# Kernel optimization log

Hardware: AMD Instinct MI355X
Metric: run time of the kernel (lower is better)

## Reference

```python
import jax, jax.numpy as jnp
import numpy as np

B_BOUND = 3.0
K = 10
SCALE_DIM = 8
TOTAL_DIM = 16
HID = 50
N = 262144
TD = TOTAL_DIM - SCALE_DIM  # transform_dim


def setup_inputs() -> dict:
    key = jax.random.key(0)
    ks = jax.random.split(key, 7)
    s = 0.1  # small init so softmax/softplus params stay well-conditioned
    return {
        "x": jax.random.normal(ks[0], (N, TOTAL_DIM), dtype=jnp.float32),
        "w0": s * jax.random.normal(ks[1], (SCALE_DIM, HID), dtype=jnp.float32),
        "b0": jnp.zeros((HID,), jnp.float32),
        "w1": s * jax.random.normal(ks[2], (HID, HID), dtype=jnp.float32),
        "b1": jnp.zeros((HID,), jnp.float32),
        "ww": s * jax.random.normal(ks[3], (HID, TD * K), dtype=jnp.float32),
        "bw": jnp.zeros((TD * K,), jnp.float32),
        "wh": s * jax.random.normal(ks[4], (HID, TD * K), dtype=jnp.float32),
        "bh": jnp.zeros((TD * K,), jnp.float32),
        "wd": s * jax.random.normal(ks[5], (HID, TD * (K - 1)), dtype=jnp.float32),
        "bd": jnp.zeros((TD * (K - 1),), jnp.float32),
    }


def _spline_forward(x, w0, b0, w1, b1, ww, bw, wh, bh, wd, bd):
    B = B_BOUND
    zd = x[:, :SCALE_DIM]          # conditioner input [N, d]
    u = x[:, SCALE_DIM:]           # values to transform [N, D]
    n, D = u.shape

    h = jnp.tanh(zd @ w0 + b0)
    h = jnp.tanh(h @ w1 + b1)

    theta_w = jax.nn.softmax((2.0 * B * (h @ ww + bw)).reshape(n, D, K), axis=-1)
    theta_h = jax.nn.softmax((2.0 * B * (h @ wh + bh)).reshape(n, D, K), axis=-1)
    theta_d = jax.nn.softplus((h @ wd + bd).reshape(n, D, K - 1))

    # Bin edges in [-B, B] via cumsum of normalized widths/heights
    xe = jnp.concatenate(
        [jnp.full((n, D, 1), -B, u.dtype), -B + 2.0 * B * jnp.cumsum(theta_w, axis=-1)], axis=-1)  # [n,D,K+1]
    ye = jnp.concatenate(
        [jnp.full((n, D, 1), -B, u.dtype), -B + 2.0 * B * jnp.cumsum(theta_h, axis=-1)], axis=-1)
    # Knot derivatives: boundary derivatives fixed to 1 (linear tails)
    ones = jnp.ones((n, D, 1), u.dtype)
    d = jnp.concatenate([ones, theta_d, ones], axis=-1)  # [n,D,K+1]

    widths = xe[..., 1:] - xe[..., :-1]
    heights = ye[..., 1:] - ye[..., :-1]

    inside = (u > -B) & (u < B)
    uc = jnp.clip(u, -B, B)
    # per-element bin search
    idx = jnp.clip(jnp.sum((uc[..., None] >= xe[..., :-1]).astype(jnp.int32), axis=-1) - 1, 0, K - 1)
    idx = idx[..., None]
    take = lambda a: jnp.take_along_axis(a, idx, axis=-1)[..., 0]

    xk, yk = take(xe[..., :-1]), take(ye[..., :-1])
    wk, hk = take(widths), take(heights)
    dk, dk1 = take(d[..., :-1]), take(d[..., 1:])

    sk = hk / wk
    xi = (uc - xk) / wk
    om = 1.0 - xi
    denom = sk + (dk1 + dk - 2.0 * sk) * xi * om
    y = yk + hk * (sk * xi * xi + dk * xi * om) / denom
    logdet = 2.0 * jnp.log(sk) + jnp.log(dk1 * xi * xi + 2.0 * sk * xi * om + dk * om * om) - 2.0 * jnp.log(denom)

    zD = jnp.where(inside, y, u)
    ld = jnp.where(inside, logdet, 0.0)
    return jnp.concatenate([zd, zD], axis=1), jnp.sum(ld)


def reference(x, w0, b0, w1, b1, ww, bw, wh, bh, wd, bd):
    return _spline_forward(x, w0, b0, w1, b1, ww, bw, wh, bh, wd, bd)
```

## Files before the change

kernel.cpp:

```cpp
#include <hip/hip_runtime.h>

#define NROWS 262144
#define KK 10
#define BB 3.0f
#define SROW 132
#define HS 84
#define SEGF16 (16 * SROW)
#define SENT 0.54132485f

typedef _Float16 v8h __attribute__((ext_vector_type(8)));
typedef _Float16 v4h __attribute__((ext_vector_type(4)));
typedef float v4f __attribute__((ext_vector_type(4)));

#define W0_OFF 0
#define W1_OFF 256
#define WC_OFF 768
#define FRAG_TOTAL 2816
#define SLOTS_OFF (FRAG_TOTAL * 4)

#if __has_builtin(__builtin_amdgcn_exp2f)
__device__ __forceinline__ float ex2(float x) { return __builtin_amdgcn_exp2f(x); }
#else
__device__ __forceinline__ float ex2(float x) { return __expf(0.6931471805599453f * x); }
#endif
#if __has_builtin(__builtin_amdgcn_rcpf)
__device__ __forceinline__ float frcp(float x) { return __builtin_amdgcn_rcpf(x); }
#else
__device__ __forceinline__ float frcp(float x) { return __fdividef(1.0f, x); }
#endif

#define LOG2E 1.4426950408889634f
#define C6 (6.0f * LOG2E)
#define CT (2.0f * LOG2E)

__device__ __forceinline__ float fast_tanh(float a) {
    const float e = ex2(CT * a);
    return fmaf(-2.0f, frcp(e + 1.0f), 1.0f);
}

__device__ __forceinline__ float softplus1(float v) {
    return fmaxf(v, 0.0f) + __logf(1.0f + ex2(-LOG2E * fabsf(v)));
}

__device__ __forceinline__ void spline_task(
    const _Float16* __restrict__ sg, int base, float ud, int g, int d,
    float* __restrict__ out, float& ldacc)
{
    float vals[32];
    #pragma unroll
    for (int blk = 0; blk < 8; ++blk) {
        const v4h p = *(const v4h*)&sg[base + blk * 4];
        vals[4 * blk + 0] = (float)p[0];
        vals[4 * blk + 1] = (float)p[1];
        vals[4 * blk + 2] = (float)p[2];
        vals[4 * blk + 3] = (float)p[3];
    }

    float mw = vals[0];
    #pragma unroll
    for (int i = 1; i < KK; ++i) mw = fmaxf(mw, vals[i]);
    const float mw8 = mw * C6;
    float sw = 0.0f;
    #pragma unroll
    for (int i = 0; i < KK; ++i) { vals[i] = ex2(fmaf(vals[i], C6, -mw8)); sw += vals[i]; }
    const float invw = frcp(sw);

    float mh = vals[10];
    #pragma unroll
    for (int i = 1; i < KK; ++i) mh = fmaxf(mh, vals[10 + i]);
    const float mh8 = mh * C6;
    float sh = 0.0f;
    #pragma unroll
    for (int i = 0; i < KK; ++i) { vals[10 + i] = ex2(fmaf(vals[10 + i], C6, -mh8)); sh += vals[10 + i]; }
    const float invh = frcp(sh);

    const float uc = fminf(fmaxf(ud, -BB), BB);
    const bool inside = (ud > -BB) && (ud < BB);

    float cw = 0.0f, ch = 0.0f;
    float xprev = -BB, yprev = -BB, rprev = SENT;
    float xk = -BB, yk = -BB, wk = 1.0f, hk2 = 1.0f, rdk = SENT, rdk1 = SENT;
    #pragma unroll
    for (int i = 0; i < KK; ++i) {
        cw += vals[i] * invw;
        ch += vals[10 + i] * invh;
        const float xnext = fmaf(6.0f, cw, -BB);
        const float ynext = fmaf(6.0f, ch, -BB);
        const float rnext = (i == KK - 1) ? SENT : vals[20 + i];
        const bool c = (i == 0) || (uc >= xprev);
        if (c) { xk = xprev; yk = yprev; wk = xnext - xprev; hk2 = ynext - yprev; rdk = rprev; rdk1 = rnext; }
        xprev = xnext; yprev = ynext; rprev = rnext;
    }
    const float dk = softplus1(rdk);
    const float dk1 = softplus1(rdk1);

    const float rwk = frcp(wk);
    const float sk = hk2 * rwk;
    const float xi = (uc - xk) * rwk;
    const float om = 1.0f - xi;
    const float denom = sk + (dk1 + dk - 2.0f * sk) * xi * om;
    const float rden = frcp(denom);
    const float ynum = sk * xi * xi + dk * xi * om;
    const float yv = yk + hk2 * ynum * rden;
    const float larg = dk1 * xi * xi + 2.0f * sk * xi * om + dk * om * om;
    const float ldet = __logf(sk * sk * larg * rden * rden);

    out[g * 16 + 8 + d] = inside ? yv : ud;
    ldacc += inside ? ldet : 0.0f;
}

__global__ __launch_bounds__(256) void nsf_prep(
    const float* __restrict__ w0, const float* __restrict__ b0,
    const float* __restrict__ w1, const float* __restrict__ b1,
    const float* __restrict__ ww, const float* __restrict__ bw,
    const float* __restrict__ wh, const float* __restrict__ bh,
    const float* __restrict__ wd, const float* __restrict__ bd,
    v8h* __restrict__ wsv, float* __restrict__ wsf)
{
    const int t = blockIdx.x * 256 + threadIdx.x;
    if (t < 64) wsf[SLOTS_OFF + t] = 0.0f;
    if (t >= FRAG_TOTAL) return;

    v8h v;
    #pragma unroll
    for (int j = 0; j < 8; ++j) v[j] = (_Float16)0.0f;

    if (t < W1_OFF) {
        const int tile = t >> 6, lane = t & 63, q = lane >> 4, n = tile * 16 + (lane & 15);
        if (n < 50) {
            #pragma unroll
            for (int j = 0; j < 8; ++j) {
                const int k = q * 8 + j;
                if (k < 8)       v[j] = (_Float16)w0[k * 50 + n];
                else if (k == 8) v[j] = (_Float16)b0[n];
            }
        }
    } else if (t < WC_OFF) {
        int p = t - W1_OFF;
        const int step = p >> 8; p &= 255;
        const int tile = p >> 6, lane = p & 63, q = lane >> 4, n = tile * 16 + (lane & 15);
        if (n < 50) {
            #pragma unroll
            for (int j = 0; j < 8; ++j) {
                const int k = step * 32 + q * 8 + j;
                if (k < 50)       v[j] = (_Float16)w1[k * 50 + n];
                else if (k == 50) v[j] = (_Float16)b1[n];
            }
        }
    } else {
        int p = t - WC_OFF;
        const int step = p >> 10; p &= 1023;
        const int tile = p >> 6, lane = p & 63, q = lane >> 4;
        const int cp = tile * 16 + (lane & 15);
        const int d = cp >> 5, jj = cp & 31;
        #pragma unroll
        for (int j = 0; j < 8; ++j) {
            const int k = step * 32 + q * 8 + j;
            float val = 0.0f;
            if (k < 50) {
                if (jj < 10)      val = ww[k * 80 + d * 10 + jj];
                else if (jj < 20) val = wh[k * 80 + d * 10 + (jj - 10)];
                else if (jj < 29) val = wd[k * 72 + d * 9 + (jj - 20)];
            } else if (k == 50) {
                if (jj < 10)      val = bw[d * 10 + jj];
                else if (jj < 20) val = bh[d * 10 + (jj - 10)];
                else if (jj < 29) val = bd[d * 9 + (jj - 20)];
            }
            v[j] = (_Float16)val;
        }
    }
    wsv[t] = v;
}

__global__ __launch_bounds__(64, 2) void nsf_main_v7(
    const float* __restrict__ x,
    const v8h* __restrict__ wsv,
    float* __restrict__ out, float* __restrict__ slots)
{
    __shared__ __align__(16) _Float16 smem[2 * SEGF16];
    const int lane = threadIdx.x & 63;
    const int q = lane >> 4, l15 = lane & 15;
    _Float16* segA = &smem[0];
    _Float16* segB = &smem[SEGF16];
    const int R0 = blockIdx.x * 32;

    const float4* xv = (const float4*)x;
    float4* ov = (float4*)out;

    const float uA0 = x[(R0 + l15) * 16 + 8 + q];
    const float uA1 = x[(R0 + l15) * 16 + 12 + q];
    const float uB0 = x[(R0 + 16 + l15) * 16 + 8 + q];
    const float uB1 = x[(R0 + 16 + l15) * 16 + 12 + q];

    {
        const int gg = R0 + (lane >> 1);
        const int part = lane & 1;
        ov[gg * 4 + part] = xv[gg * 4 + part];
    }

    v8h aA, aB;
    #pragma unroll
    for (int j = 0; j < 8; ++j) { aA[j] = (_Float16)0.0f; aB[j] = (_Float16)0.0f; }
    if (lane < 16) {
        const float4 f0 = xv[(R0 + lane) * 4 + 0];
        const float4 f1 = xv[(R0 + lane) * 4 + 1];
        aA[0] = (_Float16)f0.x; aA[1] = (_Float16)f0.y; aA[2] = (_Float16)f0.z; aA[3] = (_Float16)f0.w;
        aA[4] = (_Float16)f1.x; aA[5] = (_Float16)f1.y; aA[6] = (_Float16)f1.z; aA[7] = (_Float16)f1.w;
        const float4 g0 = xv[(R0 + 16 + lane) * 4 + 0];
        const float4 g1 = xv[(R0 + 16 + lane) * 4 + 1];
        aB[0] = (_Float16)g0.x; aB[1] = (_Float16)g0.y; aB[2] = (_Float16)g0.z; aB[3] = (_Float16)g0.w;
        aB[4] = (_Float16)g1.x; aB[5] = (_Float16)g1.y; aB[6] = (_Float16)g1.z; aB[7] = (_Float16)g1.w;
    }
    if (q == 1) { aA[0] = (_Float16)1.0f; aB[0] = (_Float16)1.0f; }

    #pragma unroll
    for (int t = 0; t < 4; ++t) {
        const v8h b = wsv[W0_OFF + t * 64 + lane];
        v4f cA = __builtin_amdgcn_mfma_f32_16x16x32_f16(b, aA, (v4f)(0.0f), 0, 0, 0);
        v4f cB = __builtin_amdgcn_mfma_f32_16x16x32_f16(b, aB, (v4f)(0.0f), 0, 0, 0);
        v4h pA, pB;
        #pragma unroll
        for (int rg = 0; rg < 4; ++rg) {
            pA[rg] = (_Float16)fast_tanh(cA[rg]);
            pB[rg] = (_Float16)fast_tanh(cB[rg]);
        }
        const int o = l15 * HS + t * 16 + q * 4;
        *(v4h*)&segA[o] = pA;
        *(v4h*)&segB[o] = pB;
    }

    v8h A0A, A1A, A0B, A1B;
    {
        const int o0 = l15 * HS + q * 8;
        const int o1 = l15 * HS + 32 + q * 8;
        const v4h a0l = *(const v4h*)&segA[o0], a0h = *(const v4h*)&segA[o0 + 4];
        const v4h a1l = *(const v4h*)&segA[o1], a1h = *(const v4h*)&segA[o1 + 4];
        const v4h b0l = *(const v4h*)&segB[o0], b0h = *(const v4h*)&segB[o0 + 4];
        const v4h b1l = *(const v4h*)&segB[o1], b1h = *(const v4h*)&segB[o1 + 4];
        #pragma unroll
        for (int j = 0; j < 4; ++j) {
            A0A[j] = a0l[j]; A0A[4 + j] = a0h[j];
            A1A[j] = a1l[j]; A1A[4 + j] = a1h[j];
            A0B[j] = b0l[j]; A0B[4 + j] = b0h[j];
            A1B[j] = b1l[j]; A1B[4 + j] = b1h[j];
        }
    }
    if (q == 2) { A1A[2] = (_Float16)1.0f; A1B[2] = (_Float16)1.0f; }
    #pragma unroll
    for (int t = 0; t < 4; ++t) {
        const v8h bf0 = wsv[W1_OFF + t * 64 + lane];
        const v8h bf1 = wsv[W1_OFF + 256 + t * 64 + lane];
        v4f cA = __builtin_amdgcn_mfma_f32_16x16x32_f16(bf0, A0A, (v4f)(0.0f), 0, 0, 0);
        cA = __builtin_amdgcn_mfma_f32_16x16x32_f16(bf1, A1A, cA, 0, 0, 0);
        v4f cB = __builtin_amdgcn_mfma_f32_16x16x32_f16(bf0, A0B, (v4f)(0.0f), 0, 0, 0);
        cB = __builtin_amdgcn_mfma_f32_16x16x32_f16(bf1, A1B, cB, 0, 0, 0);
        v4h pA, pB;
        #pragma unroll
        for (int rg = 0; rg < 4; ++rg) {
            pA[rg] = (_Float16)fast_tanh(cA[rg]);
            pB[rg] = (_Float16)fast_tanh(cB[rg]);
        }
        const int o = l15 * HS + t * 16 + q * 4;
        *(v4h*)&segA[o] = pA;
        *(v4h*)&segB[o] = pB;
    }

    {
        const int o0 = l15 * HS + q * 8;
        const int o1 = l15 * HS + 32 + q * 8;
        const v4h a0l = *(const v4h*)&segA[o0], a0h = *(const v4h*)&segA[o0 + 4];
        const v4h a1l = *(const v4h*)&segA[o1], a1h = *(const v4h*)&segA[o1 + 4];
        const v4h b0l = *(const v4h*)&segB[o0], b0h = *(const v4h*)&segB[o0 + 4];
        const v4h b1l = *(const v4h*)&segB[o1], b1h = *(const v4h*)&segB[o1 + 4];
        #pragma unroll
        for (int j = 0; j < 4; ++j) {
            A0A[j] = a0l[j]; A0A[4 + j] = a0h[j];
            A1A[j] = a1l[j]; A1A[4 + j] = a1h[j];
            A0B[j] = b0l[j]; A0B[4 + j] = b0h[j];
            A1B[j] = b1l[j]; A1B[4 + j] = b1h[j];
        }
    }
    if (q == 2) { A1A[2] = (_Float16)1.0f; A1B[2] = (_Float16)1.0f; }

    float ldacc = 0.0f;

    #pragma unroll 2
    for (int t = 0; t < 8; ++t) {
        const v8h bf0 = wsv[WC_OFF + t * 64 + lane];
        const v8h bf1 = wsv[WC_OFF + 1024 + t * 64 + lane];
        v4f cA = __builtin_amdgcn_mfma_f32_16x16x32_f16(bf0, A0A, (v4f)(0.0f), 0, 0, 0);
        cA = __builtin_amdgcn_mfma_f32_16x16x32_f16(bf1, A1A, cA, 0, 0, 0);
        v4f cB = __builtin_amdgcn_mfma_f32_16x16x32_f16(bf0, A0B, (v4f)(0.0f), 0, 0, 0);
        cB = __builtin_amdgcn_mfma_f32_16x16x32_f16(bf1, A1B, cB, 0, 0, 0);
        v4h pA, pB;
        #pragma unroll
        for (int rg = 0; rg < 4; ++rg) { pA[rg] = (_Float16)cA[rg]; pB[rg] = (_Float16)cB[rg]; }
        const int o = l15 * SROW + t * 16 + q * 4;
        *(v4h*)&segA[o] = pA;
        *(v4h*)&segB[o] = pB;
    }

    spline_task(segA, l15 * SROW + q * 32, uA0, R0 + l15, q, out, ldacc);
    spline_task(segB, l15 * SROW + q * 32, uB0, R0 + 16 + l15, q, out, ldacc);

    #pragma unroll 2
    for (int t = 8; t < 16; ++t) {
        const v8h bf0 = wsv[WC_OFF + t * 64 + lane];
        const v8h bf1 = wsv[WC_OFF + 1024 + t * 64 + lane];
        v4f cA = __builtin_amdgcn_mfma_f32_16x16x32_f16(bf0, A0A, (v4f)(0.0f), 0, 0, 0);
        cA = __builtin_amdgcn_mfma_f32_16x16x32_f16(bf1, A1A, cA, 0, 0, 0);
        v4f cB = __builtin_amdgcn_mfma_f32_16x16x32_f16(bf0, A0B, (v4f)(0.0f), 0, 0, 0);
        cB = __builtin_amdgcn_mfma_f32_16x16x32_f16(bf1, A1B, cB, 0, 0, 0);
        v4h pA, pB;
        #pragma unroll
        for (int rg = 0; rg < 4; ++rg) { pA[rg] = (_Float16)cA[rg]; pB[rg] = (_Float16)cB[rg]; }
        const int o = l15 * SROW + (t - 8) * 16 + q * 4;
        *(v4h*)&segA[o] = pA;
        *(v4h*)&segB[o] = pB;
    }

    spline_task(segA, l15 * SROW + q * 32, uA1, R0 + l15, q + 4, out, ldacc);
    spline_task(segB, l15 * SROW + q * 32, uB1, R0 + 16 + l15, q + 4, out, ldacc);

    #pragma unroll
    for (int off = 32; off > 0; off >>= 1) ldacc += __shfl_down(ldacc, off);
    if (lane == 0) atomicAdd(&slots[blockIdx.x & 63], ldacc);
}

__global__ void nsf_finish(const float* __restrict__ slots, float* __restrict__ ldp) {
    float v = slots[threadIdx.x];
    #pragma unroll
    for (int off = 32; off > 0; off >>= 1) v += __shfl_down(v, off);
    if (threadIdx.x == 0) *ldp = v;
}

extern "C" void kernel_launch(void* const* d_in, const int* in_sizes, int n_in,
                              void* d_out, int out_size, void* d_ws, size_t ws_size,
                              hipStream_t stream) {
    const float* x  = (const float*)d_in[0];
    const float* w0 = (const float*)d_in[1];
    const float* b0 = (const float*)d_in[2];
    const float* w1 = (const float*)d_in[3];
    const float* b1 = (const float*)d_in[4];
    const float* ww = (const float*)d_in[5];
    const float* bw = (const float*)d_in[6];
    const float* wh = (const float*)d_in[7];
    const float* bh = (const float*)d_in[8];
    const float* wd = (const float*)d_in[9];
    const float* bd = (const float*)d_in[10];

    float* out = (float*)d_out;
    float* ldp = out + (size_t)NROWS * 16;
    v8h* wsv = (v8h*)d_ws;
    float* wsf = (float*)d_ws;
    float* slots = wsf + SLOTS_OFF;

    hipLaunchKernelGGL(nsf_prep, dim3((FRAG_TOTAL + 255) / 256), dim3(256), 0, stream,
                       w0, b0, w1, b1, ww, bw, wh, bh, wd, bd, wsv, wsf);
    hipLaunchKernelGGL(nsf_main_v7, dim3(NROWS / 32), dim3(64), 0, stream,
                       x, wsv, out, slots);
    hipLaunchKernelGGL(nsf_finish, dim3(1), dim3(64), 0, stream, slots, ldp);
}
```

Baseline: 156.6 us.

## Keep spline-parameter MFMA outputs in registers via permuted weight columns

The column order of the packed conditioner output weights is permuted so that each lane's MFMA accumulator registers directly hold the 32 spline parameters for its own (row, dim) task. The main kernel no longer round-trips these values through shared memory as fp16 and feeds the fp32 accumulators straight into the spline evaluation. It also drops the second launch-bounds argument and fully unrolls the parameter loops. This removes LDS stores and loads plus the fp16 rounding, but increases register pressure, which may lower occupancy.

```diff
diff --git a/kernel.cpp b/kernel.cpp
--- a/kernel.cpp
+++ b/kernel.cpp
@@ -3,9 +3,8 @@
 #define NROWS 262144
 #define KK 10
 #define BB 3.0f
-#define SROW 132
 #define HS 84
-#define SEGF16 (16 * SROW)
+#define SEGH (16 * HS)
 #define SENT 0.54132485f
 
 typedef _Float16 v8h __attribute__((ext_vector_type(8)));
@@ -43,18 +42,10 @@
 }
 
 __device__ __forceinline__ void spline_task(
-    const _Float16* __restrict__ sg, int base, float ud, int g, int d,
+    const float* __restrict__ vals, float ud, int g, int d,
     float* __restrict__ out, float& ldacc)
 {
-    float vals[32];
-    #pragma unroll
-    for (int blk = 0; blk < 8; ++blk) {
-        const v4h p = *(const v4h*)&sg[base + blk * 4];
-        vals[4 * blk + 0] = (float)p[0];
-        vals[4 * blk + 1] = (float)p[1];
-        vals[4 * blk + 2] = (float)p[2];
-        vals[4 * blk + 3] = (float)p[3];
-    }
+    float ew[KK], eh[KK];
 
     float mw = vals[0];
     #pragma unroll
@@ -62,7 +53,7 @@
     const float mw8 = mw * C6;
     float sw = 0.0f;
     #pragma unroll
-    for (int i = 0; i < KK; ++i) { vals[i] = ex2(fmaf(vals[i], C6, -mw8)); sw += vals[i]; }
+    for (int i = 0; i < KK; ++i) { ew[i] = ex2(fmaf(vals[i], C6, -mw8)); sw += ew[i]; }
     const float invw = frcp(sw);
 
     float mh = vals[10];
@@ -71,7 +62,7 @@
     const float mh8 = mh * C6;
     float sh = 0.0f;
     #pragma unroll
-    for (int i = 0; i < KK; ++i) { vals[10 + i] = ex2(fmaf(vals[10 + i], C6, -mh8)); sh += vals[10 + i]; }
+    for (int i = 0; i < KK; ++i) { eh[i] = ex2(fmaf(vals[10 + i], C6, -mh8)); sh += eh[i]; }
     const float invh = frcp(sh);
 
     const float uc = fminf(fmaxf(ud, -BB), BB);
@@ -82,8 +73,8 @@
     float xk = -BB, yk = -BB, wk = 1.0f, hk2 = 1.0f, rdk = SENT, rdk1 = SENT;
     #pragma unroll
     for (int i = 0; i < KK; ++i) {
-        cw += vals[i] * invw;
-        ch += vals[10 + i] * invh;
+        cw += ew[i] * invw;
+        ch += eh[i] * invh;
         const float xnext = fmaf(6.0f, cw, -BB);
         const float ynext = fmaf(6.0f, ch, -BB);
         const float rnext = (i == KK - 1) ? SENT : vals[20 + i];
@@ -152,7 +143,8 @@
         const int step = p >> 10; p &= 1023;
         const int tile = p >> 6, lane = p & 63, q = lane >> 4;
         const int cp = tile * 16 + (lane & 15);
-        const int d = cp >> 5, jj = cp & 31;
+        const int d  = ((cp >> 7) << 2) | ((cp >> 2) & 3);
+        const int jj = (((cp >> 4) & 7) << 2) | (cp & 3);
         #pragma unroll
         for (int j = 0; j < 8; ++j) {
             const int k = step * 32 + q * 8 + j;
@@ -172,16 +164,16 @@
     wsv[t] = v;
 }
 
-__global__ __launch_bounds__(64, 2) void nsf_main_v7(
+__global__ __launch_bounds__(64) void nsf_main_v9(
     const float* __restrict__ x,
     const v8h* __restrict__ wsv,
     float* __restrict__ out, float* __restrict__ slots)
 {
-    __shared__ __align__(16) _Float16 smem[2 * SEGF16];
+    __shared__ __align__(16) _Float16 smem[6272];
     const int lane = threadIdx.x & 63;
     const int q = lane >> 4, l15 = lane & 15;
     _Float16* segA = &smem[0];
-    _Float16* segB = &smem[SEGF16];
+    _Float16* segB = &smem[SEGH];
     const int R0 = blockIdx.x * 32;
 
     const float4* xv = (const float4*)x;
@@ -283,8 +275,9 @@
     if (q == 2) { A1A[2] = (_Float16)1.0f; A1B[2] = (_Float16)1.0f; }
 
     float ldacc = 0.0f;
-
-    #pragma unroll 2
+    float vA[32], vB[32];
+
+    #pragma unroll
     for (int t = 0; t < 8; ++t) {
         const v8h bf0 = wsv[WC_OFF + t * 64 + lane];
         const v8h bf1 = wsv[WC_OFF + 1024 + t * 64 + lane];
@@ -292,18 +285,13 @@
         cA = __builtin_amdgcn_mfma_f32_16x16x32_f16(bf1, A1A, cA, 0, 0, 0);
         v4f cB = __builtin_amdgcn_mfma_f32_16x16x32_f16(bf0, A0B, (v4f)(0.0f), 0, 0, 0);
         cB = __builtin_amdgcn_mfma_f32_16x16x32_f16(bf1, A1B, cB, 0, 0, 0);
-        v4h pA, pB;
-        #pragma unroll
-        for (int rg = 0; rg < 4; ++rg) { pA[rg] = (_Float16)cA[rg]; pB[rg] = (_Float16)cB[rg]; }
-        const int o = l15 * SROW + t * 16 + q * 4;
-        *(v4h*)&segA[o] = pA;
-        *(v4h*)&segB[o] = pB;
-    }
-
-    spline_task(segA, l15 * SROW + q * 32, uA0, R0 + l15, q, out, ldacc);
-    spline_task(segB, l15 * SROW + q * 32, uB0, R0 + 16 + l15, q, out, ldacc);
-
-    #pragma unroll 2
+        #pragma unroll
+        for (int rg = 0; rg < 4; ++rg) { vA[4 * t + rg] = cA[rg]; vB[4 * t + rg] = cB[rg]; }
+    }
+    spline_task(vA, uA0, R0 + l15, q, out, ldacc);
+    spline_task(vB, uB0, R0 + 16 + l15, q, out, ldacc);
+
+    #pragma unroll
     for (int t = 8; t < 16; ++t) {
         const v8h bf0 = wsv[WC_OFF + t * 64 + lane];
         const v8h bf1 = wsv[WC_OFF + 1024 + t * 64 + lane];
@@ -311,16 +299,11 @@
         cA = __builtin_amdgcn_mfma_f32_16x16x32_f16(bf1, A1A, cA, 0, 0, 0);
         v4f cB = __builtin_amdgcn_mfma_f32_16x16x32_f16(bf0, A0B, (v4f)(0.0f), 0, 0, 0);
         cB = __builtin_amdgcn_mfma_f32_16x16x32_f16(bf1, A1B, cB, 0, 0, 0);
-        v4h pA, pB;
-        #pragma unroll
-        for (int rg = 0; rg < 4; ++rg) { pA[rg] = (_Float16)cA[rg]; pB[rg] = (_Float16)cB[rg]; }
-        const int o = l15 * SROW + (t - 8) * 16 + q * 4;
-        *(v4h*)&segA[o] = pA;
-        *(v4h*)&segB[o] = pB;
-    }
-
-    spline_task(segA, l15 * SROW + q * 32, uA1, R0 + l15, q + 4, out, ldacc);
-    spline_task(segB, l15 * SROW + q * 32, uB1, R0 + 16 + l15, q + 4, out, ldacc);
+        #pragma unroll
+        for (int rg = 0; rg < 4; ++rg) { vA[4 * (t - 8) + rg] = cA[rg]; vB[4 * (t - 8) + rg] = cB[rg]; }
+    }
+    spline_task(vA, uA1, R0 + l15, q + 4, out, ldacc);
+    spline_task(vB, uB1, R0 + 16 + l15, q + 4, out, ldacc);
 
     #pragma unroll
     for (int off = 32; off > 0; off >>= 1) ldacc += __shfl_down(ldacc, off);
@@ -357,7 +340,7 @@
 
     hipLaunchKernelGGL(nsf_prep, dim3((FRAG_TOTAL + 255) / 256), dim3(256), 0, stream,
                        w0, b0, w1, b1, ww, bw, wh, bh, wd, bd, wsv, wsf);
-    hipLaunchKernelGGL(nsf_main_v7, dim3(NROWS / 32), dim3(64), 0, stream,
+    hipLaunchKernelGGL(nsf_main_v9, dim3(NROWS / 32), dim3(64), 0, stream,
                        x, wsv, out, slots);
     hipLaunchKernelGGL(nsf_finish, dim3(1), dim3(64), 0, stream, slots, ldp);
 }
```

Measured after the change: 162.1 us. 1.04x slower.

## Make main kernel persistent over 4 tiles with register prefetch of next tile

Applied to the files above, without the earlier changes.

The main kernel now launches a fixed 2048 single-wave blocks, each looping over four 32-row tiles strided by the grid size. While one tile is computed, the x loads for the next tile are issued into registers so global latency overlaps the MFMA and spline work. The launch-bounds minimum-occupancy hint is dropped, which lets the compiler use more registers. The prefetch registers may lower occupancy, and fewer blocks means less latency hiding across waves.

```diff
diff --git a/kernel.cpp b/kernel.cpp
--- a/kernel.cpp
+++ b/kernel.cpp
@@ -7,6 +7,7 @@
 #define HS 84
 #define SEGF16 (16 * SROW)
 #define SENT 0.54132485f
+#define NBLK 2048
 
 typedef _Float16 v8h __attribute__((ext_vector_type(8)));
 typedef _Float16 v4h __attribute__((ext_vector_type(4)));
@@ -172,7 +173,7 @@
     wsv[t] = v;
 }
 
-__global__ __launch_bounds__(64, 2) void nsf_main_v7(
+__global__ __launch_bounds__(64) void nsf_main_v11(
     const float* __restrict__ x,
     const v8h* __restrict__ wsv,
     float* __restrict__ out, float* __restrict__ slots)
@@ -182,145 +183,162 @@
     const int q = lane >> 4, l15 = lane & 15;
     _Float16* segA = &smem[0];
     _Float16* segB = &smem[SEGF16];
-    const int R0 = blockIdx.x * 32;
+    const int pr = lane >> 1, pc = lane & 1;
 
     const float4* xv = (const float4*)x;
     float4* ov = (float4*)out;
 
-    const float uA0 = x[(R0 + l15) * 16 + 8 + q];
-    const float uA1 = x[(R0 + l15) * 16 + 12 + q];
-    const float uB0 = x[(R0 + 16 + l15) * 16 + 8 + q];
-    const float uB1 = x[(R0 + 16 + l15) * 16 + 12 + q];
-
-    {
-        const int gg = R0 + (lane >> 1);
-        const int part = lane & 1;
-        ov[gg * 4 + part] = xv[gg * 4 + part];
+    float4 ph_n = make_float4(0.f, 0.f, 0.f, 0.f);
+    float uA0_n = 0.f, uA1_n = 0.f, uB0_n = 0.f, uB1_n = 0.f;
+    float4 f0_n = ph_n, f1_n = ph_n, g0_n = ph_n, g1_n = ph_n;
+
+    auto PREF = [&](int p) {
+        const int R0 = p * 32;
+        ph_n  = xv[(R0 + pr) * 4 + pc];
+        uA0_n = x[(R0 + l15) * 16 + 8 + q];
+        uA1_n = x[(R0 + l15) * 16 + 12 + q];
+        uB0_n = x[(R0 + 16 + l15) * 16 + 8 + q];
+        uB1_n = x[(R0 + 16 + l15) * 16 + 12 + q];
+        if (lane < 16) {
+            f0_n = xv[(R0 + lane) * 4 + 0];
+            f1_n = xv[(R0 + lane) * 4 + 1];
+            g0_n = xv[(R0 + 16 + lane) * 4 + 0];
+            g1_n = xv[(R0 + 16 + lane) * 4 + 1];
+        }
+    };
+
+    PREF(blockIdx.x);
+    float ldacc = 0.0f;
+
+    #pragma unroll 1
+    for (int it = 0; it < 4; ++it) {
+        const int pcur = it * NBLK + blockIdx.x;
+        const int R0 = pcur * 32;
+        const float4 phc = ph_n;
+        const float uA0 = uA0_n, uA1 = uA1_n, uB0 = uB0_n, uB1 = uB1_n;
+        const float4 f0 = f0_n, f1 = f1_n, g0 = g0_n, g1 = g1_n;
+        if (it < 3) PREF((it + 1) * NBLK + blockIdx.x);
+
+        ov[(R0 + pr) * 4 + pc] = phc;
+
+        v8h aA, aB;
+        #pragma unroll
+        for (int j = 0; j < 8; ++j) { aA[j] = (_Float16)0.0f; aB[j] = (_Float16)0.0f; }
+        if (lane < 16) {
+            aA[0] = (_Float16)f0.x; aA[1] = (_Float16)f0.y; aA[2] = (_Float16)f0.z; aA[3] = (_Float16)f0.w;
+            aA[4] = (_Float16)f1.x; aA[5] = (_Float16)f1.y; aA[6] = (_Float16)f1.z; aA[7] = (_Float16)f1.w;
+            aB[0] = (_Float16)g0.x; aB[1] = (_Float16)g0.y; aB[2] = (_Float16)g0.z; aB[3] = (_Float16)g0.w;
+            aB[4] = (_Float16)g1.x; aB[5] = (_Float16)g1.y; aB[6] = (_Float16)g1.z; aB[7] = (_Float16)g1.w;
+        }
+        if (q == 1) { aA[0] = (_Float16)1.0f; aB[0] = (_Float16)1.0f; }
+
+        #pragma unroll
+        for (int t = 0; t < 4; ++t) {
+            const v8h b = wsv[W0_OFF + t * 64 + lane];
+            v4f cA = __builtin_amdgcn_mfma_f32_16x16x32_f16(b, aA, (v4f)(0.0f), 0, 0, 0);
+            v4f cB = __builtin_amdgcn_mfma_f32_16x16x32_f16(b, aB, (v4f)(0.0f), 0, 0, 0);
+            v4h pA, pB;
+            #pragma unroll
+            for (int rg = 0; rg < 4; ++rg) {
+                pA[rg] = (_Float16)fast_tanh(cA[rg]);
+                pB[rg] = (_Float16)fast_tanh(cB[rg]);
+            }
+            const int o = l15 * HS + t * 16 + q * 4;
+            *(v4h*)&segA[o] = pA;
+            *(v4h*)&segB[o] = pB;
+        }
+
+        v8h A0A, A1A, A0B, A1B;
+        {
+            const int o0 = l15 * HS + q * 8;
+            const int o1 = l15 * HS + 32 + q * 8;
+            const v4h a0l = *(const v4h*)&segA[o0], a0h = *(const v4h*)&segA[o0 + 4];
+            const v4h a1l = *(const v4h*)&segA[o1], a1h = *(const v4h*)&segA[o1 + 4];
+            const v4h b0l = *(const v4h*)&segB[o0], b0h = *(const v4h*)&segB[o0 + 4];
+            const v4h b1l = *(const v4h*)&segB[o1], b1h = *(const v4h*)&segB[o1 + 4];
+            #pragma unroll
+            for (int j = 0; j < 4; ++j) {
+                A0A[j] = a0l[j]; A0A[4 + j] = a0h[j];
+                A1A[j] = a1l[j]; A1A[4 + j] = a1h[j];
+                A0B[j] = b0l[j]; A0B[4 + j] = b0h[j];
+                A1B[j] = b1l[j]; A1B[4 + j] = b1h[j];
+            }
+        }
+        if (q == 2) { A1A[2] = (_Float16)1.0f; A1B[2] = (_Float16)1.0f; }
+        #pragma unroll
+        for (int t = 0; t < 4; ++t) {
+            const v8h bf0 = wsv[W1_OFF + t * 64 + lane];
+            const v8h bf1 = wsv[W1_OFF + 256 + t * 64 + lane];
+            v4f cA = __builtin_amdgcn_mfma_f32_16x16x32_f16(bf0, A0A, (v4f)(0.0f), 0, 0, 0);
+            cA = __builtin_amdgcn_mfma_f32_16x16x32_f16(bf1, A1A, cA, 0, 0, 0);
+            v4f cB = __builtin_amdgcn_mfma_f32_16x16x32_f16(bf0, A0B, (v4f)(0.0f), 0, 0, 0);
+            cB = __builtin_amdgcn_mfma_f32_16x16x32_f16(bf1, A1B, cB, 0, 0, 0);
+            v4h pA, pB;
+            #pragma unroll
+            for (int rg = 0; rg < 4; ++rg) {
+                pA[rg] = (_Float16)fast_tanh(cA[rg]);
+                pB[rg] = (_Float16)fast_tanh(cB[rg]);
+            }
+            const int o = l15 * HS + t * 16 + q * 4;
+            *(v4h*)&segA[o] = pA;
+            *(v4h*)&segB[o] = pB;
+        }
+
+        {
+            const int o0 = l15 * HS + q * 8;
+            const int o1 = l15 * HS + 32 + q * 8;
+            const v4h a0l = *(const v4h*)&segA[o0], a0h = *(const v4h*)&segA[o0 + 4];
+            const v4h a1l = *(const v4h*)&segA[o1], a1h = *(const v4h*)&segA[o1 + 4];
+            const v4h b0l = *(const v4h*)&segB[o0], b0h = *(const v4h*)&segB[o0 + 4];
+            const v4h b1l = *(const v4h*)&segB[o1], b1h = *(const v4h*)&segB[o1 + 4];
+            #pragma unroll
+            for (int j = 0; j < 4; ++j) {
+                A0A[j] = a0l[j]; A0A[4 + j] = a0h[j];
+                A1A[j] = a1l[j]; A1A[4 + j] = a1h[j];
+                A0B[j] = b0l[j]; A0B[4 + j] = b0h[j];
+                A1B[j] = b1l[j]; A1B[4 + j] = b1h[j];
+            }
+        }
+        if (q == 2) { A1A[2] = (_Float16)1.0f; A1B[2] = (_Float16)1.0f; }
+
+        #pragma unroll 2
+        for (int t = 0; t < 8; ++t) {
+            const v8h bf0 = wsv[WC_OFF + t * 64 + lane];
+            const v8h bf1 = wsv[WC_OFF + 1024 + t * 64 + lane];
+            v4f cA = __builtin_amdgcn_mfma_f32_16x16x32_f16(bf0, A0A, (v4f)(0.0f), 0, 0, 0);
+            cA = __builtin_amdgcn_mfma_f32_16x16x32_f16(bf1, A1A, cA, 0, 0, 0);
+            v4f cB = __builtin_amdgcn_mfma_f32_16x16x32_f16(bf0, A0B, (v4f)(0.0f), 0, 0, 0);
+            cB = __builtin_amdgcn_mfma_f32_16x16x32_f16(bf1, A1B, cB, 0, 0, 0);
+            v4h pA, pB;
+            #pragma unroll
+            for (int rg = 0; rg < 4; ++rg) { pA[rg] = (_Float16)cA[rg]; pB[rg] = (_Float16)cB[rg]; }
+            const int o = l15 * SROW + t * 16 + q * 4;
+            *(v4h*)&segA[o] = pA;
+            *(v4h*)&segB[o] = pB;
+        }
+
+        spline_task(segA, l15 * SROW + q * 32, uA0, R0 + l15, q, out, ldacc);
+        spline_task(segB, l15 * SROW + q * 32, uB0, R0 + 16 + l15, q, out, ldacc);
+
+        #pragma unroll 2
+        for (int t = 8; t < 16; ++t) {
+            const v8h bf0 = wsv[WC_OFF + t * 64 + lane];
+            const v8h bf1 = wsv[WC_OFF + 1024 + t * 64 + lane];
+            v4f cA = __builtin_amdgcn_mfma_f32_16x16x32_f16(bf0, A0A, (v4f)(0.0f), 0, 0, 0);
+            cA = __builtin_amdgcn_mfma_f32_16x16x32_f16(bf1, A1A, cA, 0, 0, 0);
+            v4f cB = __builtin_amdgcn_mfma_f32_16x16x32_f16(bf0, A0B, (v4f)(0.0f), 0, 0, 0);
+            cB = __builtin_amdgcn_mfma_f32_16x16x32_f16(bf1, A1B, cB, 0, 0, 0);
+            v4h pA, pB;
+            #pragma unroll
+            for (int rg = 0; rg < 4; ++rg) { pA[rg] = (_Float16)cA[rg]; pB[rg] = (_Float16)cB[rg]; }
+            const int o = l15 * SROW + (t - 8) * 16 + q * 4;
+            *(v4h*)&segA[o] = pA;
+            *(v4h*)&segB[o] = pB;
+        }
+
+        spline_task(segA, l15 * SROW + q * 32, uA1, R0 + l15, q + 4, out, ldacc);
+        spline_task(segB, l15 * SROW + q * 32, uB1, R0 + 16 + l15, q + 4, out, ldacc);
     }
-
-    v8h aA, aB;
-    #pragma unroll
-    for (int j = 0; j < 8; ++j) { aA[j] = (_Float16)0.0f; aB[j] = (_Float16)0.0f; }
-    if (lane < 16) {
-        const float4 f0 = xv[(R0 + lane) * 4 + 0];
-        const float4 f1 = xv[(R0 + lane) * 4 + 1];
-        aA[0] = (_Float16)f0.x; aA[1] = (_Float16)f0.y; aA[2] = (_Float16)f0.z; aA[3] = (_Float16)f0.w;
-        aA[4] = (_Float16)f1.x; aA[5] = (_Float16)f1.y; aA[6] = (_Float16)f1.z; aA[7] = (_Float16)f1.w;
-        const float4 g0 = xv[(R0 + 16 + lane) * 4 + 0];
-        const float4 g1 = xv[(R0 + 16 + lane) * 4 + 1];
-        aB[0] = (_Float16)g0.x; aB[1] = (_Float16)g0.y; aB[2] = (_Float16)g0.z; aB[3] = (_Float16)g0.w;
-        aB[4] = (_Float16)g1.x; aB[5] = (_Float16)g1.y; aB[6] = (_Float16)g1.z; aB[7] = (_Float16)g1.w;
-    }
-    if (q == 1) { aA[0] = (_Float16)1.0f; aB[0] = (_Float16)1.0f; }
-
-    #pragma unroll
-    for (int t = 0; t < 4; ++t) {
-        const v8h b = wsv[W0_OFF + t * 64 + lane];
-        v4f cA = __builtin_amdgcn_mfma_f32_16x16x32_f16(b, aA, (v4f)(0.0f), 0, 0, 0);
-        v4f cB = __builtin_amdgcn_mfma_f32_16x16x32_f16(b, aB, (v4f)(0.0f), 0, 0, 0);
-        v4h pA, pB;
-        #pragma unroll
-        for (int rg = 0; rg < 4; ++rg) {
-            pA[rg] = (_Float16)fast_tanh(cA[rg]);
-            pB[rg] = (_Float16)fast_tanh(cB[rg]);
-        }
-        const int o = l15 * HS + t * 16 + q * 4;
-        *(v4h*)&segA[o] = pA;
-        *(v4h*)&segB[o] = pB;
-    }
-
-    v8h A0A, A1A, A0B, A1B;
-    {
-        const int o0 = l15 * HS + q * 8;
-        const int o1 = l15 * HS + 32 + q * 8;
-        const v4h a0l = *(const v4h*)&segA[o0], a0h = *(const v4h*)&segA[o0 + 4];
-        const v4h a1l = *(const v4h*)&segA[o1], a1h = *(const v4h*)&segA[o1 + 4];
-        const v4h b0l = *(const v4h*)&segB[o0], b0h = *(const v4h*)&segB[o0 + 4];
-        const v4h b1l = *(const v4h*)&segB[o1], b1h = *(const v4h*)&segB[o1 + 4];
-        #pragma unroll
-        for (int j = 0; j < 4; ++j) {
-            A0A[j] = a0l[j]; A0A[4 + j] = a0h[j];
-            A1A[j] = a1l[j]; A1A[4 + j] = a1h[j];
-            A0B[j] = b0l[j]; A0B[4 + j] = b0h[j];
-            A1B[j] = b1l[j]; A1B[4 + j] = b1h[j];
-        }
-    }
-    if (q == 2) { A1A[2] = (_Float16)1.0f; A1B[2] = (_Float16)1.0f; }
-    #pragma unroll
-    for (int t = 0; t < 4; ++t) {
-        const v8h bf0 = wsv[W1_OFF + t * 64 + lane];
-        const v8h bf1 = wsv[W1_OFF + 256 + t * 64 + lane];
-        v4f cA = __builtin_amdgcn_mfma_f32_16x16x32_f16(bf0, A0A, (v4f)(0.0f), 0, 0, 0);
-        cA = __builtin_amdgcn_mfma_f32_16x16x32_f16(bf1, A1A, cA, 0, 0, 0);
-        v4f cB = __builtin_amdgcn_mfma_f32_16x16x32_f16(bf0, A0B, (v4f)(0.0f), 0, 0, 0);
-        cB = __builtin_amdgcn_mfma_f32_16x16x32_f16(bf1, A1B, cB, 0, 0, 0);
-        v4h pA, pB;
-        #pragma unroll
-        for (int rg = 0; rg < 4; ++rg) {
-            pA[rg] = (_Float16)fast_tanh(cA[rg]);
-            pB[rg] = (_Float16)fast_tanh(cB[rg]);
-        }
-        const int o = l15 * HS + t * 16 + q * 4;
-        *(v4h*)&segA[o] = pA;
-        *(v4h*)&segB[o] = pB;
-    }
-
-    {
-        const int o0 = l15 * HS + q * 8;
-        const int o1 = l15 * HS + 32 + q * 8;
-        const v4h a0l = *(const v4h*)&segA[o0], a0h = *(const v4h*)&segA[o0 + 4];
-        const v4h a1l = *(const v4h*)&segA[o1], a1h = *(const v4h*)&segA[o1 + 4];
-        const v4h b0l = *(const v4h*)&segB[o0], b0h = *(const v4h*)&segB[o0 + 4];
-        const v4h b1l = *(const v4h*)&segB[o1], b1h = *(const v4h*)&segB[o1 + 4];
-        #pragma unroll
-        for (int j = 0; j < 4; ++j) {
-            A0A[j] = a0l[j]; A0A[4 + j] = a0h[j];
-            A1A[j] = a1l[j]; A1A[4 + j] = a1h[j];
-            A0B[j] = b0l[j]; A0B[4 + j] = b0h[j];
-            A1B[j] = b1l[j]; A1B[4 + j] = b1h[j];
-        }
-    }
-    if (q == 2) { A1A[2] = (_Float16)1.0f; A1B[2] = (_Float16)1.0f; }
-
-    float ldacc = 0.0f;
-
-    #pragma unroll 2
-    for (int t = 0; t < 8; ++t) {
-        const v8h bf0 = wsv[WC_OFF + t * 64 + lane];
-        const v8h bf1 = wsv[WC_OFF + 1024 + t * 64 + lane];
-        v4f cA = __builtin_amdgcn_mfma_f32_16x16x32_f16(bf0, A0A, (v4f)(0.0f), 0, 0, 0);
-        cA = __builtin_amdgcn_mfma_f32_16x16x32_f16(bf1, A1A, cA, 0, 0, 0);
-        v4f cB = __builtin_amdgcn_mfma_f32_16x16x32_f16(bf0, A0B, (v4f)(0.0f), 0, 0, 0);
-        cB = __builtin_amdgcn_mfma_f32_16x16x32_f16(bf1, A1B, cB, 0, 0, 0);
-        v4h pA, pB;
-        #pragma unroll
-        for (int rg = 0; rg < 4; ++rg) { pA[rg] = (_Float16)cA[rg]; pB[rg] = (_Float16)cB[rg]; }
-        const int o = l15 * SROW + t * 16 + q * 4;
-        *(v4h*)&segA[o] = pA;
-        *(v4h*)&segB[o] = pB;
-    }
-
-    spline_task(segA, l15 * SROW + q * 32, uA0, R0 + l15, q, out, ldacc);
-    spline_task(segB, l15 * SROW + q * 32, uB0, R0 + 16 + l15, q, out, ldacc);
-
-    #pragma unroll 2
-    for (int t = 8; t < 16; ++t) {
-        const v8h bf0 = wsv[WC_OFF + t * 64 + lane];
-        const v8h bf1 = wsv[WC_OFF + 1024 + t * 64 + lane];
-        v4f cA = __builtin_amdgcn_mfma_f32_16x16x32_f16(bf0, A0A, (v4f)(0.0f), 0, 0, 0);
-        cA = __builtin_amdgcn_mfma_f32_16x16x32_f16(bf1, A1A, cA, 0, 0, 0);
-        v4f cB = __builtin_amdgcn_mfma_f32_16x16x32_f16(bf0, A0B, (v4f)(0.0f), 0, 0, 0);
-        cB = __builtin_amdgcn_mfma_f32_16x16x32_f16(bf1, A1B, cB, 0, 0, 0);
-        v4h pA, pB;
-        #pragma unroll
-        for (int rg = 0; rg < 4; ++rg) { pA[rg] = (_Float16)cA[rg]; pB[rg] = (_Float16)cB[rg]; }
-        const int o = l15 * SROW + (t - 8) * 16 + q * 4;
-        *(v4h*)&segA[o] = pA;
-        *(v4h*)&segB[o] = pB;
-    }
-
-    spline_task(segA, l15 * SROW + q * 32, uA1, R0 + l15, q + 4, out, ldacc);
-    spline_task(segB, l15 * SROW + q * 32, uB1, R0 + 16 + l15, q + 4, out, ldacc);
 
     #pragma unroll
     for (int off = 32; off > 0; off >>= 1) ldacc += __shfl_down(ldacc, off);
@@ -357,7 +375,7 @@
 
     hipLaunchKernelGGL(nsf_prep, dim3((FRAG_TOTAL + 255) / 256), dim3(256), 0, stream,
                        w0, b0, w1, b1, ww, bw, wh, bh, wd, bd, wsv, wsf);
-    hipLaunchKernelGGL(nsf_main_v7, dim3(NROWS / 32), dim3(64), 0, stream,
+    hipLaunchKernelGGL(nsf_main_v11, dim3(NBLK), dim3(64), 0, stream,
                        x, wsv, out, slots);
     hipLaunchKernelGGL(nsf_finish, dim3(1), dim3(64), 0, stream, slots, ldp);
 }
```

Result: faster. 139.1 us (-11.2%).
